# Performance work log

Measured on AMD Instinct MI355X. Metric: run time of the kernel, lower is better.

## Reference

```python
import jax, jax.numpy as jnp
import numpy as np

EPS = 1e-3  # BatchNorm eps (eval mode: running_mean=0, running_var=1)
GRID_D, GRID_H, GRID_W, GRID_C = 10, 400, 352, 128


def bn_last(x, g, b):
    # BatchNorm1d eval over last (channel) axis
    return x * (g / jnp.sqrt(1.0 + EPS)) + b


def bn_ch(x, g, b):
    # BatchNorm3d eval, channel axis 1 of NCDHW
    s = (g / jnp.sqrt(1.0 + EPS)).reshape(1, -1, 1, 1, 1)
    return x * s + b.reshape(1, -1, 1, 1, 1)


def vfe_layer(x, W, g, b):
    # x: [N, T, Cin] -> [N, T, 2*units]
    h = jnp.einsum('ntc,uc->ntu', x, W)
    h = jax.nn.relu(bn_last(h, g, b))
    agg = jnp.max(h, axis=1, keepdims=True)          # [N,1,units]
    return jnp.concatenate([h, jnp.broadcast_to(agg, h.shape)], axis=2)


def pad3(x, p):
    # torch ConstantPad3d order: (Wl, Wr, Hl, Hr, Dl, Dr); x is NCDHW
    return jnp.pad(x, ((0, 0), (0, 0), (p[4], p[5]), (p[2], p[3]), (p[0], p[1])))


def conv3d(x, w, stride):
    return jax.lax.conv_general_dilated(
        x, w, window_strides=stride, padding='VALID',
        dimension_numbers=('NCDHW', 'OIDHW', 'NCDHW'))


def setup_inputs() -> dict:
    key = jax.random.key(0)
    ks = jax.random.split(key, 12)
    N, T = 20000, 35
    features = jax.random.normal(ks[0], (N, T, 4), jnp.float32)
    num_voxels = jax.random.randint(ks[1], (N,), 1, T + 1, jnp.int32)
    cb = jnp.zeros((N, 1), jnp.int32)
    cd = jax.random.randint(ks[2], (N, 1), 0, GRID_D, jnp.int32)
    ch = jax.random.randint(ks[3], (N, 1), 0, GRID_H, jnp.int32)
    cw = jax.random.randint(ks[4], (N, 1), 0, GRID_W, jnp.int32)
    coors = jnp.concatenate([cb, cd, ch, cw], axis=1)

    def lin(k, o, i):
        return jax.random.normal(k, (o, i), jnp.float32) / np.sqrt(i)

    def cw3(k, o, i):
        return jax.random.normal(k, (o, i, 3, 3, 3), jnp.float32) / np.sqrt(i * 27)

    return {
        'features': features, 'num_voxels': num_voxels, 'coors': coors, 'batch_size': 1,
        'w_vfe1': lin(ks[5], 16, 7), 'g_vfe1': jnp.ones(16), 'b_vfe1': jnp.zeros(16),
        'w_vfe2': lin(ks[6], 64, 32), 'g_vfe2': jnp.ones(64), 'b_vfe2': jnp.zeros(64),
        'w_lin': lin(ks[7], 128, 128), 'g_lin': jnp.ones(128), 'b_lin': jnp.zeros(128),
        'w_c1': cw3(ks[8], 64, 128), 'g_c1': jnp.ones(64), 'b_c1': jnp.zeros(64),
        'w_c2': cw3(ks[9], 64, 64), 'g_c2': jnp.ones(64), 'b_c2': jnp.zeros(64),
        'w_c3': cw3(ks[10], 64, 64), 'g_c3': jnp.ones(64), 'b_c3': jnp.zeros(64),
    }


def reference(features, num_voxels, coors, batch_size,
              w_vfe1, g_vfe1, b_vfe1, w_vfe2, g_vfe2, b_vfe2,
              w_lin, g_lin, b_lin,
              w_c1, g_c1, b_c1, w_c2, g_c2, b_c2, w_c3, g_c3, b_c3):
    # --- VoxelFeatureExtractor ---
    nv = num_voxels.astype(features.dtype)[:, None, None]
    points_mean = features[:, :, :3].sum(axis=1, keepdims=True) / nv
    rel = features[:, :, :3] - points_mean
    f = jnp.concatenate([features, rel], axis=-1)                 # [N,T,7]
    T = f.shape[1]
    mask = (jnp.arange(T)[None, :] < num_voxels[:, None]).astype(f.dtype)[..., None]
    x = vfe_layer(f, w_vfe1, g_vfe1, b_vfe1) * mask               # [N,T,32]
    x = vfe_layer(x, w_vfe2, g_vfe2, b_vfe2) * mask               # [N,T,128]
    x = jnp.einsum('ntc,uc->ntu', x, w_lin)
    x = jax.nn.relu(bn_last(x, g_lin, b_lin)) * mask
    voxelwise = jnp.max(x, axis=1)                                # [N,128]

    # --- MiddleExtractor: scatter_nd + 3D convs ---
    grid = jnp.zeros((batch_size, GRID_D, GRID_H, GRID_W, GRID_C), f.dtype)
    grid = grid.at[coors[:, 0], coors[:, 1], coors[:, 2], coors[:, 3]].set(voxelwise)
    r = grid.transpose(0, 4, 1, 2, 3)                             # NCDHW [1,128,10,400,352]
    r = pad3(r, (1, 1, 1, 1, 1, 1))
    r = jax.nn.relu(bn_ch(conv3d(r, w_c1, (2, 1, 1)), g_c1, b_c1))  # [1,64,5,400,352]
    r = pad3(r, (1, 1, 1, 1, 0, 0))
    r = jax.nn.relu(bn_ch(conv3d(r, w_c2, (1, 1, 1)), g_c2, b_c2))  # [1,64,3,400,352]
    r = pad3(r, (1, 1, 1, 1, 1, 1))
    r = jax.nn.relu(bn_ch(conv3d(r, w_c3, (2, 1, 1)), g_c3, b_c3))  # [1,64,2,400,352]
    Nb, C, D, H, W = r.shape
    return r.reshape(Nb, C * D, H, W)                             # [1,128,400,352]
```

## Files before the change

### kernel.cpp

```cpp
#include <hip/hip_runtime.h>
#include <hip/hip_bf16.h>

#define BNC 0.99950037f
#define GH 400
#define GW 352

typedef __bf16 bf16_t;
typedef __bf16 bf16x8 __attribute__((ext_vector_type(8)));
typedef __bf16 bf16x4 __attribute__((ext_vector_type(4)));
typedef float f32x4 __attribute__((ext_vector_type(4)));

__global__ void k_winner(const int* __restrict__ coors, int* __restrict__ winner, int N) {
    int i = blockIdx.x * 256 + threadIdx.x;
    if (i >= N) return;
    int d = coors[i*4+1], h = coors[i*4+2], w = coors[i*4+3];
    atomicMax(&winner[(d*GH + h)*GW + w], i);
}

__global__ void k_tr_w(const float* __restrict__ w, float* __restrict__ wt, int CI, int CO) {
    int idx = blockIdx.x * 256 + threadIdx.x;
    int total = 27 * CI * CO;
    if (idx >= total) return;
    int j   = idx & 3;
    int t1  = idx >> 2;
    int co  = t1 % CO;
    int t2  = t1 / CO;
    int ci4 = t2 % (CI/4);
    int tap = t2 / (CI/4);
    int ci  = ci4*4 + j;
    wt[idx] = w[(co*CI + ci)*27 + tap];
}

__global__ void k_tr_lin(const float* __restrict__ wl, float* __restrict__ WT) {
    int idx = blockIdx.x * 256 + threadIdx.x;
    if (idx >= 16384) return;
    int u = idx & 127, c = idx >> 7;
    WT[c*128 + u] = wl[u*128 + c];
}

__global__ void k_prep(const float* __restrict__ g, const float* __restrict__ b,
                       float* __restrict__ out) {
    int i = threadIdx.x;
    if (i < 64)       out[i] = g[i] * BNC;
    else if (i < 128) out[i] = b[i-64];
}

__global__ void k_packw(const float* __restrict__ w, bf16_t* __restrict__ wh,
                        bf16_t* __restrict__ wlo) {
    int i = blockIdx.x * 256 + threadIdx.x;
    if (i >= 13824) return;
    int lane = i & 63, ct = (i >> 6) & 3, s = i >> 8;
    int tap = s >> 1, h = s & 1;
    int kg = lane >> 4, wl = lane & 15;
    int co = ct*16 + wl;
    #pragma unroll
    for (int j = 0; j < 8; ++j) {
        int ci = h*32 + kg*8 + j;
        float v = w[(co*64 + ci)*27 + tap];
        bf16_t hi = (bf16_t)v;
        wh[(long)i*8 + j]  = hi;
        wlo[(long)i*8 + j] = (bf16_t)(v - (float)hi);
    }
}

__global__ __launch_bounds__(256) void k_vfe(
    const float* __restrict__ feats, const int* __restrict__ nvox,
    const float* __restrict__ w1, const float* __restrict__ g1g, const float* __restrict__ b1g,
    const float* __restrict__ w2g, const float* __restrict__ g2g, const float* __restrict__ b2g,
    const float* __restrict__ WT, const float* __restrict__ glg, const float* __restrict__ blg,
    float* __restrict__ voxelwise, int N)
{
    __shared__ float S[2][4672];
    __shared__ float W1s[16*8];
    __shared__ float SG1[16], SB1[16];

    int tid = threadIdx.x;
    int v   = tid >> 7, lt = tid & 127;
    int vox = blockIdx.x*2 + v;
    if (vox >= N) vox = N - 1;
    int nv  = nvox[vox];

    float* F     = &S[v][0];
    float* X1    = &S[v][280];
    float* X2    = &S[v][980];
    float* RED   = &S[v][3360];
    float* AGG1  = &S[v][4384];
    float* AGG2  = &S[v][4400];
    float* Y2B   = &S[v][4464];
    float* YB    = &S[v][4528];
    float* MEANS = &S[v][4656];

    const float* fsrc = feats + (long)vox * 140;
    for (int idx = lt; idx < 140; idx += 128) { int t = idx>>2, c = idx&3; F[t*8+c] = fsrc[idx]; }
    if (lt < 35) F[lt*8+7] = 0.f;
    if (tid < 112) { int u = tid/7, c = tid - u*7; W1s[u*8+c] = w1[tid]; }
    if (tid < 16)  { W1s[tid*8+7] = 0.f; SG1[tid] = g1g[tid]*BNC; SB1[tid] = b1g[tid]; }
    __syncthreads();

    if (lt < 3) {
        float s = 0.f;
        for (int t = 0; t < 35; ++t) s += F[t*8 + lt];
        MEANS[lt] = s / (float)nv;
    }
    __syncthreads();
    for (int idx = lt; idx < 105; idx += 128) { int t = idx/3, c = idx - t*3; F[t*8+4+c] = F[t*8+c] - MEANS[c]; }
    __syncthreads();

    {
        const float4* Ff4  = (const float4*)F;
        const float4* W1f4 = (const float4*)W1s;
        for (int idx = lt; idx < 560; idx += 128) {
            int t = idx >> 4, u = idx & 15;
            float4 a0 = Ff4[t*2], a1 = Ff4[t*2+1];
            float4 b0 = W1f4[u*2], b1v = W1f4[u*2+1];
            float a = a0.x*b0.x + a0.y*b0.y + a0.z*b0.z + a0.w*b0.w
                    + a1.x*b1v.x + a1.y*b1v.y + a1.z*b1v.z + a1.w*b1v.w;
            X1[t*20+u] = fmaxf(a*SG1[u] + SB1[u], 0.f);
        }
    }
    __syncthreads();
    if (lt < 16) {
        float m = 0.f;
        for (int t = 0; t < 35; ++t) m = fmaxf(m, X1[t*20+lt]);
        AGG1[lt] = m;
    }
    __syncthreads();
    if (lt < 64) {
        const float4* wsrc = (const float4*)(w2g + lt*32 + 16);
        const float4* A1f4 = (const float4*)AGG1;
        float a = 0.f;
        #pragma unroll
        for (int q = 0; q < 4; ++q) {
            float4 w4 = wsrc[q], x4 = A1f4[q];
            a += x4.x*w4.x + x4.y*w4.y + x4.z*w4.z + x4.w*w4.w;
        }
        Y2B[lt] = a;
    }
    __syncthreads();

    {
        int u = lt & 63, tg = lt >> 6;
        float w2r[16];
        const float4* wsrc = (const float4*)(w2g + u*32);
        #pragma unroll
        for (int q = 0; q < 4; ++q) {
            float4 w4 = wsrc[q];
            w2r[q*4] = w4.x; w2r[q*4+1] = w4.y; w2r[q*4+2] = w4.z; w2r[q*4+3] = w4.w;
        }
        float su = g2g[u]*BNC, bu = b2g[u];
        float yb2 = Y2B[u];
        float lm = (nv < 35) ? fmaxf(bu, 0.f) : 0.f;
        for (int t = tg; t < nv; t += 2) {
            const float4* xr = (const float4*)(X1 + t*20);
            float a = yb2;
            #pragma unroll
            for (int q = 0; q < 4; ++q) {
                float4 x4 = xr[q];
                a += x4.x*w2r[q*4] + x4.y*w2r[q*4+1] + x4.z*w2r[q*4+2] + x4.w*w2r[q*4+3];
            }
            float h = fmaxf(a*su + bu, 0.f);
            X2[t*68 + u] = h;
            lm = fmaxf(lm, h);
        }
        RED[tg*64 + u] = lm;
    }
    __syncthreads();
    if (lt < 64) AGG2[lt] = fmaxf(RED[lt], RED[64+lt]);
    __syncthreads();
    {
        float a = 0.f;
        for (int c = 0; c < 64; ++c) a = fmaf(AGG2[c], WT[(64 + c)*128 + lt], a);
        YB[lt] = a;
    }
    __syncthreads();

    {
        int ug = lt & 15, tg4 = lt >> 4;
        int u0 = ug * 8;
        int kmax = (nv > tg4) ? ((nv - tg4 + 7) >> 3) : 0;
        float acc[5][8];
        #pragma unroll
        for (int k = 0; k < 5; ++k)
            #pragma unroll
            for (int j = 0; j < 8; ++j) acc[k][j] = 0.f;

        const float4* X2f4 = (const float4*)X2;
        const float4* WTf4 = (const float4*)WT;
        for (int c4 = 0; c4 < 16; ++c4) {
            float4 wv[8];
            #pragma unroll
            for (int cc = 0; cc < 4; ++cc) {
                wv[cc*2]   = WTf4[(c4*4+cc)*32 + ug*2];
                wv[cc*2+1] = WTf4[(c4*4+cc)*32 + ug*2 + 1];
            }
            #pragma unroll
            for (int k = 0; k < 5; ++k) {
                if (k < kmax) {
                    int t = tg4 + (k << 3);
                    float4 x4 = X2f4[t*17 + c4];
                    #pragma unroll
                    for (int cc = 0; cc < 4; ++cc) {
                        float xs = (cc == 0) ? x4.x : (cc == 1) ? x4.y : (cc == 2) ? x4.z : x4.w;
                        acc[k][0] = fmaf(xs, wv[cc*2].x,   acc[k][0]);
                        acc[k][1] = fmaf(xs, wv[cc*2].y,   acc[k][1]);
                        acc[k][2] = fmaf(xs, wv[cc*2].z,   acc[k][2]);
                        acc[k][3] = fmaf(xs, wv[cc*2].w,   acc[k][3]);
                        acc[k][4] = fmaf(xs, wv[cc*2+1].x, acc[k][4]);
                        acc[k][5] = fmaf(xs, wv[cc*2+1].y, acc[k][5]);
                        acc[k][6] = fmaf(xs, wv[cc*2+1].z, acc[k][6]);
                        acc[k][7] = fmaf(xs, wv[cc*2+1].w, acc[k][7]);
                    }
                }
            }
        }
        float4 g0 = *(const float4*)(glg + u0), g1v = *(const float4*)(glg + u0 + 4);
        float4 b0 = *(const float4*)(blg + u0), b1v = *(const float4*)(blg + u0 + 4);
        float4 y0 = *(const float4*)(YB + u0),  y1v = *(const float4*)(YB + u0 + 4);
        float sg[8] = {g0.x*BNC, g0.y*BNC, g0.z*BNC, g0.w*BNC,
                       g1v.x*BNC, g1v.y*BNC, g1v.z*BNC, g1v.w*BNC};
        float sb[8] = {b0.x, b0.y, b0.z, b0.w, b1v.x, b1v.y, b1v.z, b1v.w};
        float yv[8] = {y0.x, y0.y, y0.z, y0.w, y1v.x, y1v.y, y1v.z, y1v.w};
        float m[8];
        #pragma unroll
        for (int j = 0; j < 8; ++j) m[j] = 0.f;
        #pragma unroll
        for (int k = 0; k < 5; ++k) {
            if (k < kmax) {
                #pragma unroll
                for (int j = 0; j < 8; ++j)
                    m[j] = fmaxf(m[j], fmaxf((acc[k][j] + yv[j])*sg[j] + sb[j], 0.f));
            }
        }
        #pragma unroll
        for (int j = 0; j < 8; ++j) RED[tg4*128 + u0 + j] = m[j];
    }
    __syncthreads();
    {
        float m = RED[lt];
        #pragma unroll
        for (int r = 1; r < 8; ++r) m = fmaxf(m, RED[r*128 + lt]);
        voxelwise[(long)vox*128 + lt] = m;
    }
}

__global__ __launch_bounds__(256) void k_gat1(
    const float4* __restrict__ voxf4, const int* __restrict__ winner,
    const float4* __restrict__ Wt1, bf16_t* __restrict__ accH,
    bf16_t* __restrict__ accL, const float* __restrict__ gact,
    int h_lo, int AR)
{
    int r  = blockIdx.y;
    int oh = h_lo + r;
    if ((unsigned)oh >= (unsigned)GH) return;
    int doo = blockIdx.z;
    int w0  = blockIdx.x * 32;

    __shared__ int sList[306];
    __shared__ int sCnt;
    __shared__ float4 sF[32][32];

    int t = threadIdx.x;
    if (t == 0) sCnt = 0;
    __syncthreads();
    for (int idx = t; idx < 306; idx += 256) {
        int x = idx % 34, q = idx / 34;
        int kd = q / 3, kh = q - kd*3;
        int dp = doo*2 + kd - 1;
        int hp = oh + kh - 1;
        int wp = w0 - 1 + x;
        if ((unsigned)dp < 10u && (unsigned)hp < (unsigned)GH && (unsigned)wp < (unsigned)GW) {
            int v = winner[(dp*GH + hp)*GW + wp];
            if (v >= 0) {
                int p = atomicAdd(&sCnt, 1);
                sList[p] = (v << 10) | (kd << 8) | (kh << 6) | x;
            }
        }
    }
    __syncthreads();
    int cnt = sCnt;

    int co = t & 63, wv = t >> 6;
    int ibase = wv*8;
    float acc[8];
    #pragma unroll
    for (int i = 0; i < 8; ++i) acc[i] = 0.f;

    for (int c0 = 0; c0 < cnt; c0 += 32) {
        int nch = min(32, cnt - c0);
        __syncthreads();
        for (int idx = t; idx < nch*32; idx += 256) {
            int slot = idx >> 5, c = idx & 31;
            int widx = sList[c0 + slot] >> 10;
            sF[slot][c] = voxf4[(long)widx*32 + c];
        }
        __syncthreads();
        for (int e = 0; e < nch; ++e) {
            int ent = sList[c0 + e];
            int x = ent & 63, kh = (ent >> 6) & 3, kd = (ent >> 8) & 3;
            #pragma unroll
            for (int kw = 0; kw < 3; ++kw) {
                int i = x - kw;
                if (i >= ibase && i < ibase + 8) {
                    const float4* wb = Wt1 + (long)(kd*9 + kh*3 + kw)*2048 + co;
                    float a = 0.f;
                    #pragma unroll 4
                    for (int c4 = 0; c4 < 32; ++c4) {
                        float4 wq = wb[c4*64];
                        float4 f4 = sF[e][c4];
                        a += f4.x*wq.x + f4.y*wq.y + f4.z*wq.z + f4.w*wq.w;
                    }
                    int j = i - ibase;
                    #pragma unroll
                    for (int j8 = 0; j8 < 8; ++j8)
                        if (j8 == j) acc[j8] += a;
                }
            }
        }
    }

    float g = gact[co], b = gact[64 + co];
    long rowb = ((long)doo*AR + r)*GW + w0;
    #pragma unroll
    for (int i = 0; i < 8; ++i) {
        float rr = fmaxf(acc[i]*g + b, 0.f);
        bf16_t hi = (bf16_t)rr;
        long idx = (rowb + ibase + i)*64 + co;
        accH[idx] = hi;
        accL[idx] = (bf16_t)(rr - (float)hi);
    }
}

__global__ __launch_bounds__(256) void k_convm(
    const bf16_t* __restrict__ srcH, const bf16_t* __restrict__ srcL,
    int src_h0, long src_dpitch,
    float* __restrict__ dstF, bf16_t* __restrict__ dstH, bf16_t* __restrict__ dstL,
    int dst_h0, long sC, long sD, long sH,
    const bf16_t* __restrict__ wph, const bf16_t* __restrict__ wpl,
    const float* __restrict__ gout, const float* __restrict__ bout,
    int D_in, int d_stride, int d_pad, int y0)
{
    int oh = y0 + (int)blockIdx.y;
    if ((unsigned)oh >= (unsigned)GH) return;

    __shared__ __align__(16) char smem[17408];
    bf16_t* sAh = (bf16_t*)smem;
    bf16_t* sAl = (bf16_t*)(smem + 8448);
    float*  sOut = (float*)smem;

    int t = threadIdx.x;
    int lane = t & 63, wv = t >> 6;
    int wl = lane & 15, kg = lane >> 4;
    int mh = wv >> 1, cth = wv & 1;
    int w0 = (int)blockIdx.x * 64;
    int od = (int)blockIdx.z;

    f32x4 acc[2][2];
    #pragma unroll
    for (int a = 0; a < 2; ++a)
        #pragma unroll
        for (int b = 0; b < 2; ++b) acc[a][b] = (f32x4){0.f, 0.f, 0.f, 0.f};

    const bf16x8* WH = (const bf16x8*)wph;
    const bf16x8* WL = (const bf16x8*)wpl;

    for (int kd = 0; kd < 3; ++kd) {
        int dp = od*d_stride + kd - d_pad;
        if (dp < 0 || dp >= D_in) continue;
        const bf16_t* sdbH = srcH + dp*src_dpitch;
        const bf16_t* sdbL = srcL + dp*src_dpitch;
        for (int kh = 0; kh < 3; ++kh) {
            int hp = oh + kh - 1;
            bool vh = ((unsigned)hp < (unsigned)GH);
            long rowoff = (long)(hp - src_h0) * (GW*64);
            __syncthreads();
            for (int c = t; c < 1056; c += 256) {
                int pl = (c >= 528) ? 1 : 0;
                int cc = c - (pl << 9) - (pl << 4);
                int g = cc / 66, w = cc - g*66;
                int gw = w0 - 1 + w;
                bf16x8 vv;
                if (vh && (unsigned)gw < (unsigned)GW) {
                    const bf16_t* plane = pl ? sdbL : sdbH;
                    vv = *(const bf16x8*)(plane + rowoff + (long)gw*64 + g*8);
                } else {
                    #pragma unroll
                    for (int e = 0; e < 8; ++e) vv[e] = (bf16_t)0.f;
                }
                bf16_t* dstl = pl ? sAl : sAh;
                *(bf16x8*)&dstl[(g*66 + w)*8] = vv;
            }
            __syncthreads();
            #pragma unroll
            for (int h = 0; h < 2; ++h) {
                #pragma unroll
                for (int kw = 0; kw < 3; ++kw) {
                    int s = ((kd*3 + kh)*3 + kw)*2 + h;
                    long fb = (long)(s*4 + cth*2)*64 + lane;
                    bf16x8 B0h = WH[fb],      B0l = WL[fb];
                    bf16x8 B1h = WH[fb + 64], B1l = WL[fb + 64];
                    #pragma unroll
                    for (int mt = 0; mt < 2; ++mt) {
                        int ai = ((h*4 + kg)*66 + (mh*2 + mt)*16 + kw + wl)*8;
                        bf16x8 Ah = *(const bf16x8*)&sAh[ai];
                        bf16x8 Al = *(const bf16x8*)&sAl[ai];
                        acc[mt][0] = __builtin_amdgcn_mfma_f32_16x16x32_bf16(Ah, B0h, acc[mt][0], 0, 0, 0);
                        acc[mt][0] = __builtin_amdgcn_mfma_f32_16x16x32_bf16(Ah, B0l, acc[mt][0], 0, 0, 0);
                        acc[mt][0] = __builtin_amdgcn_mfma_f32_16x16x32_bf16(Al, B0h, acc[mt][0], 0, 0, 0);
                        acc[mt][1] = __builtin_amdgcn_mfma_f32_16x16x32_bf16(Ah, B1h, acc[mt][1], 0, 0, 0);
                        acc[mt][1] = __builtin_amdgcn_mfma_f32_16x16x32_bf16(Ah, B1l, acc[mt][1], 0, 0, 0);
                        acc[mt][1] = __builtin_amdgcn_mfma_f32_16x16x32_bf16(Al, B1h, acc[mt][1], 0, 0, 0);
                    }
                }
            }
        }
    }

    float so[2], bo[2];
    #pragma unroll
    for (int ct = 0; ct < 2; ++ct) {
        int co = (cth*2 + ct)*16 + wl;
        so[ct] = gout[co]*BNC; bo[ct] = bout[co];
    }
    if (dstF) {
        #pragma unroll
        for (int mt = 0; mt < 2; ++mt) {
            int ow = w0 + (mh*2 + mt)*16 + kg*4;
            if (ow < GW) {
                #pragma unroll
                for (int ct = 0; ct < 2; ++ct) {
                    int co = (cth*2 + ct)*16 + wl;
                    f32x4 r;
                    #pragma unroll
                    for (int e = 0; e < 4; ++e)
                        r[e] = fmaxf(acc[mt][ct][e]*so[ct] + bo[ct], 0.f);
                    *(f32x4*)&dstF[(long)co*sC + (long)od*sD + (long)(oh - dst_h0)*sH + ow] = r;
                }
            }
        }
    } else {
        __syncthreads();
        #pragma unroll
        for (int mt = 0; mt < 2; ++mt)
            #pragma unroll
            for (int ct = 0; ct < 2; ++ct) {
                int co = (cth*2 + ct)*16 + wl;
                #pragma unroll
                for (int e = 0; e < 4; ++e) {
                    int owl = (mh*2 + mt)*16 + kg*4 + e;
                    sOut[owl*68 + co] = fmaxf(acc[mt][ct][e]*so[ct] + bo[ct], 0.f);
                }
            }
        __syncthreads();
        for (int f = t; f < 1024; f += 256) {
            int w = f >> 4, c4 = f & 15;
            if (w0 + w < GW) {
                float4 v = *(const float4*)&sOut[w*68 + c4*4];
                long base = (long)od*sD + (long)(oh - dst_h0)*sH + (long)(w0 + w)*64 + c4*4;
                bf16_t h0 = (bf16_t)v.x, h1 = (bf16_t)v.y, h2 = (bf16_t)v.z, h3 = (bf16_t)v.w;
                bf16x4 hv; hv[0]=h0; hv[1]=h1; hv[2]=h2; hv[3]=h3;
                bf16x4 lv;
                lv[0]=(bf16_t)(v.x-(float)h0); lv[1]=(bf16_t)(v.y-(float)h1);
                lv[2]=(bf16_t)(v.z-(float)h2); lv[3]=(bf16_t)(v.w-(float)h3);
                *(bf16x4*)&dstH[base] = hv;
                *(bf16x4*)&dstL[base] = lv;
            }
        }
    }
}

extern "C" void kernel_launch(void* const* d_in, const int* in_sizes, int n_in,
                              void* d_out, int out_size, void* d_ws, size_t ws_size,
                              hipStream_t stream)
{
    const float* feats = (const float*)d_in[0];
    const int*   nvox  = (const int*)d_in[1];
    const int*   coors = (const int*)d_in[2];
    const float* w1  = (const float*)d_in[4];
    const float* g1  = (const float*)d_in[5];
    const float* b1  = (const float*)d_in[6];
    const float* w2  = (const float*)d_in[7];
    const float* g2  = (const float*)d_in[8];
    const float* b2  = (const float*)d_in[9];
    const float* wl  = (const float*)d_in[10];
    const float* gl  = (const float*)d_in[11];
    const float* bl  = (const float*)d_in[12];
    const float* wc1 = (const float*)d_in[13];
    const float* gc1 = (const float*)d_in[14];
    const float* bc1 = (const float*)d_in[15];
    const float* wc2 = (const float*)d_in[16];
    const float* gc2 = (const float*)d_in[17];
    const float* bc2 = (const float*)d_in[18];
    const float* wc3 = (const float*)d_in[19];
    const float* gc3 = (const float*)d_in[20];
    const float* bc3 = (const float*)d_in[21];

    int N = in_sizes[1];

    auto al = [](size_t b) { return (b + 255) & ~(size_t)255; };

    size_t winB = al((size_t)10*GH*GW*4);
    size_t voxB = al((size_t)N*128*4);
    size_t w1B  = al((size_t)27*128*64*4);
    size_t wlB  = al((size_t)128*128*4);
    size_t wpB  = al((size_t)13824*8*2);
    int NS = 20;
    const int cand[8] = {1, 2, 4, 5, 8, 10, 16, 20};
    for (int k = 0; k < 8; ++k) {
        int ns = cand[k], sh = 400/ns, ar = sh + 4, xr = sh + 2;
        size_t tot = 2*al((size_t)5*ar*GW*64*2) + 2*al((size_t)3*xr*GW*64*2)
                   + winB + voxB + w1B + wlB + 4*wpB + 4096;
        if (tot + (1<<16) <= ws_size) { NS = ns; break; }
    }
    int SH = 400/NS, AR = SH + 4, XR = SH + 2;

    char* ws = (char*)d_ws;
    size_t off = 0;
    auto alloc = [&](size_t bytes) -> void* {
        void* p = ws + off; off += al(bytes); return p;
    };
    size_t accB = (size_t)5*AR*GW*64*2;
    size_t actB = (size_t)3*XR*GW*64*2;
    bf16_t* accH   = (bf16_t*)alloc(accB);
    bf16_t* accL   = (bf16_t*)alloc(accB);
    bf16_t* actH   = (bf16_t*)alloc(actB);
    bf16_t* actL   = (bf16_t*)alloc(actB);
    int*    winner = (int*)alloc((size_t)10*GH*GW*4);
    float*  voxw   = (float*)alloc((size_t)N*128*4);
    float*  wt1    = (float*)alloc((size_t)27*128*64*4);
    float*  wtl    = (float*)alloc((size_t)128*128*4);
    bf16_t* wp2h   = (bf16_t*)alloc(wpB);
    bf16_t* wp2l   = (bf16_t*)alloc(wpB);
    bf16_t* wp3h   = (bf16_t*)alloc(wpB);
    bf16_t* wp3l   = (bf16_t*)alloc(wpB);
    float*  gact   = (float*)alloc(256*4);

    hipMemsetAsync(winner, 0xFF, (size_t)10*GH*GW*4, stream);

    k_tr_w<<<(27*128*64 + 255)/256, 256, 0, stream>>>(wc1, wt1, 128, 64);
    k_tr_lin<<<64, 256, 0, stream>>>(wl, wtl);
    k_packw<<<54, 256, 0, stream>>>(wc2, wp2h, wp2l);
    k_packw<<<54, 256, 0, stream>>>(wc3, wp3h, wp3l);
    k_prep<<<1, 256, 0, stream>>>(gc1, bc1, gact);

    k_winner<<<(N + 255)/256, 256, 0, stream>>>(coors, winner, N);
    k_vfe<<<(N + 1)/2, 256, 0, stream>>>(feats, nvox, w1, g1, b1, w2, g2, b2,
                                         wtl, gl, bl, voxw, N);

    for (int s = 0; s < NS; ++s) {
        k_gat1<<<dim3(11, AR, 5), 256, 0, stream>>>(
            (const float4*)voxw, winner, (const float4*)wt1,
            accH, accL, gact, s*SH - 2, AR);
        k_convm<<<dim3(6, SH + 2, 3), 256, 0, stream>>>(
            accH, accL, s*SH - 2, (long)AR*GW*64,
            nullptr, actH, actL, s*SH - 1, 0L, (long)XR*GW*64, (long)GW*64,
            wp2h, wp2l, gc2, bc2,
            5, 1, 0, s*SH - 1);
        k_convm<<<dim3(6, SH, 2), 256, 0, stream>>>(
            actH, actL, s*SH - 1, (long)XR*GW*64,
            (float*)d_out, nullptr, nullptr, 0, (long)2*GH*GW, (long)GH*GW, (long)GW,
            wp3h, wp3l, gc3, bc3,
            3, 2, 1, s*SH);
    }
}
```

Measured before the change: 1.083 ms.

## Compute two output rows per conv block and use one voxel per VFE block

Measured after the change: 1.018 ms. 6.0% less time.

```diff
diff --git a/kernel.cpp b/kernel.cpp
--- a/kernel.cpp
+++ b/kernel.cpp
@@ -63,53 +63,49 @@
     }
 }
 
-__global__ __launch_bounds__(256) void k_vfe(
+__global__ __launch_bounds__(128) void k_vfe(
     const float* __restrict__ feats, const int* __restrict__ nvox,
     const float* __restrict__ w1, const float* __restrict__ g1g, const float* __restrict__ b1g,
     const float* __restrict__ w2g, const float* __restrict__ g2g, const float* __restrict__ b2g,
     const float* __restrict__ WT, const float* __restrict__ glg, const float* __restrict__ blg,
-    float* __restrict__ voxelwise, int N)
+    float* __restrict__ voxelwise)
 {
-    __shared__ float S[2][4672];
+    __shared__ float F[35*8];
     __shared__ float W1s[16*8];
     __shared__ float SG1[16], SB1[16];
+    __shared__ float X1[35*20];
+    __shared__ float X2[35*68];
+    __shared__ float RED[4*128];
+    __shared__ float AGG1[16];
+    __shared__ float AGG2[64];
+    __shared__ float Y2B[64];
+    __shared__ float YB[128];
+    __shared__ float MEANS[3];
 
     int tid = threadIdx.x;
-    int v   = tid >> 7, lt = tid & 127;
-    int vox = blockIdx.x*2 + v;
-    if (vox >= N) vox = N - 1;
+    int vox = blockIdx.x;
     int nv  = nvox[vox];
 
-    float* F     = &S[v][0];
-    float* X1    = &S[v][280];
-    float* X2    = &S[v][980];
-    float* RED   = &S[v][3360];
-    float* AGG1  = &S[v][4384];
-    float* AGG2  = &S[v][4400];
-    float* Y2B   = &S[v][4464];
-    float* YB    = &S[v][4528];
-    float* MEANS = &S[v][4656];
-
     const float* fsrc = feats + (long)vox * 140;
-    for (int idx = lt; idx < 140; idx += 128) { int t = idx>>2, c = idx&3; F[t*8+c] = fsrc[idx]; }
-    if (lt < 35) F[lt*8+7] = 0.f;
+    for (int idx = tid; idx < 140; idx += 128) { int t = idx>>2, c = idx&3; F[t*8+c] = fsrc[idx]; }
+    if (tid < 35) F[tid*8+7] = 0.f;
     if (tid < 112) { int u = tid/7, c = tid - u*7; W1s[u*8+c] = w1[tid]; }
     if (tid < 16)  { W1s[tid*8+7] = 0.f; SG1[tid] = g1g[tid]*BNC; SB1[tid] = b1g[tid]; }
     __syncthreads();
 
-    if (lt < 3) {
+    if (tid < 3) {
         float s = 0.f;
-        for (int t = 0; t < 35; ++t) s += F[t*8 + lt];
-        MEANS[lt] = s / (float)nv;
-    }
-    __syncthreads();
-    for (int idx = lt; idx < 105; idx += 128) { int t = idx/3, c = idx - t*3; F[t*8+4+c] = F[t*8+c] - MEANS[c]; }
+        for (int t = 0; t < 35; ++t) s += F[t*8 + tid];
+        MEANS[tid] = s / (float)nv;
+    }
+    __syncthreads();
+    for (int idx = tid; idx < 105; idx += 128) { int t = idx/3, c = idx - t*3; F[t*8+4+c] = F[t*8+c] - MEANS[c]; }
     __syncthreads();
 
     {
         const float4* Ff4  = (const float4*)F;
         const float4* W1f4 = (const float4*)W1s;
-        for (int idx = lt; idx < 560; idx += 128) {
+        for (int idx = tid; idx < 560; idx += 128) {
             int t = idx >> 4, u = idx & 15;
             float4 a0 = Ff4[t*2], a1 = Ff4[t*2+1];
             float4 b0 = W1f4[u*2], b1v = W1f4[u*2+1];
@@ -119,14 +115,14 @@
         }
     }
     __syncthreads();
-    if (lt < 16) {
+    if (tid < 16) {
         float m = 0.f;
-        for (int t = 0; t < 35; ++t) m = fmaxf(m, X1[t*20+lt]);
-        AGG1[lt] = m;
-    }
-    __syncthreads();
-    if (lt < 64) {
-        const float4* wsrc = (const float4*)(w2g + lt*32 + 16);
+        for (int t = 0; t < 35; ++t) m = fmaxf(m, X1[t*20+tid]);
+        AGG1[tid] = m;
+    }
+    __syncthreads();
+    if (tid < 64) {
+        const float4* wsrc = (const float4*)(w2g + tid*32 + 16);
         const float4* A1f4 = (const float4*)AGG1;
         float a = 0.f;
         #pragma unroll
@@ -134,12 +130,12 @@
             float4 w4 = wsrc[q], x4 = A1f4[q];
             a += x4.x*w4.x + x4.y*w4.y + x4.z*w4.z + x4.w*w4.w;
         }
-        Y2B[lt] = a;
+        Y2B[tid] = a;
     }
     __syncthreads();
 
     {
-        int u = lt & 63, tg = lt >> 6;
+        int u = tid & 63, tg = tid >> 6;
         float w2r[16];
         const float4* wsrc = (const float4*)(w2g + u*32);
         #pragma unroll
@@ -165,81 +161,74 @@
         RED[tg*64 + u] = lm;
     }
     __syncthreads();
-    if (lt < 64) AGG2[lt] = fmaxf(RED[lt], RED[64+lt]);
+    if (tid < 64) AGG2[tid] = fmaxf(RED[tid], RED[64+tid]);
     __syncthreads();
     {
         float a = 0.f;
-        for (int c = 0; c < 64; ++c) a = fmaf(AGG2[c], WT[(64 + c)*128 + lt], a);
-        YB[lt] = a;
+        for (int c = 0; c < 64; ++c) a = fmaf(AGG2[c], WT[(64 + c)*128 + tid], a);
+        YB[tid] = a;
     }
     __syncthreads();
 
     {
-        int ug = lt & 15, tg4 = lt >> 4;
-        int u0 = ug * 8;
-        int kmax = (nv > tg4) ? ((nv - tg4 + 7) >> 3) : 0;
-        float acc[5][8];
-        #pragma unroll
-        for (int k = 0; k < 5; ++k)
-            #pragma unroll
-            for (int j = 0; j < 8; ++j) acc[k][j] = 0.f;
+        int ug = tid & 31, tg4 = tid >> 5;
+        int u0 = ug * 4;
+        int kmax = (nv > tg4) ? ((nv - tg4 + 3) >> 2) : 0;
+        float acc[9][4];
+        #pragma unroll
+        for (int k = 0; k < 9; ++k)
+            #pragma unroll
+            for (int j = 0; j < 4; ++j) acc[k][j] = 0.f;
 
         const float4* X2f4 = (const float4*)X2;
         const float4* WTf4 = (const float4*)WT;
         for (int c4 = 0; c4 < 16; ++c4) {
-            float4 wv[8];
-            #pragma unroll
-            for (int cc = 0; cc < 4; ++cc) {
-                wv[cc*2]   = WTf4[(c4*4+cc)*32 + ug*2];
-                wv[cc*2+1] = WTf4[(c4*4+cc)*32 + ug*2 + 1];
-            }
-            #pragma unroll
-            for (int k = 0; k < 5; ++k) {
+            float4 wv[4];
+            #pragma unroll
+            for (int cc = 0; cc < 4; ++cc)
+                wv[cc] = WTf4[(c4*4+cc)*32 + ug];
+            #pragma unroll
+            for (int k = 0; k < 9; ++k) {
                 if (k < kmax) {
-                    int t = tg4 + (k << 3);
+                    int t = tg4 + (k << 2);
                     float4 x4 = X2f4[t*17 + c4];
                     #pragma unroll
                     for (int cc = 0; cc < 4; ++cc) {
                         float xs = (cc == 0) ? x4.x : (cc == 1) ? x4.y : (cc == 2) ? x4.z : x4.w;
-                        acc[k][0] = fmaf(xs, wv[cc*2].x,   acc[k][0]);
-                        acc[k][1] = fmaf(xs, wv[cc*2].y,   acc[k][1]);
-                        acc[k][2] = fmaf(xs, wv[cc*2].z,   acc[k][2]);
-                        acc[k][3] = fmaf(xs, wv[cc*2].w,   acc[k][3]);
-                        acc[k][4] = fmaf(xs, wv[cc*2+1].x, acc[k][4]);
-                        acc[k][5] = fmaf(xs, wv[cc*2+1].y, acc[k][5]);
-                        acc[k][6] = fmaf(xs, wv[cc*2+1].z, acc[k][6]);
-                        acc[k][7] = fmaf(xs, wv[cc*2+1].w, acc[k][7]);
+                        acc[k][0] = fmaf(xs, wv[cc].x, acc[k][0]);
+                        acc[k][1] = fmaf(xs, wv[cc].y, acc[k][1]);
+                        acc[k][2] = fmaf(xs, wv[cc].z, acc[k][2]);
+                        acc[k][3] = fmaf(xs, wv[cc].w, acc[k][3]);
                     }
                 }
             }
         }
-        float4 g0 = *(const float4*)(glg + u0), g1v = *(const float4*)(glg + u0 + 4);
-        float4 b0 = *(const float4*)(blg + u0), b1v = *(const float4*)(blg + u0 + 4);
-        float4 y0 = *(const float4*)(YB + u0),  y1v = *(const float4*)(YB + u0 + 4);
-        float sg[8] = {g0.x*BNC, g0.y*BNC, g0.z*BNC, g0.w*BNC,
-                       g1v.x*BNC, g1v.y*BNC, g1v.z*BNC, g1v.w*BNC};
-        float sb[8] = {b0.x, b0.y, b0.z, b0.w, b1v.x, b1v.y, b1v.z, b1v.w};
-        float yv[8] = {y0.x, y0.y, y0.z, y0.w, y1v.x, y1v.y, y1v.z, y1v.w};
-        float m[8];
-        #pragma unroll
-        for (int j = 0; j < 8; ++j) m[j] = 0.f;
-        #pragma unroll
-        for (int k = 0; k < 5; ++k) {
+        float4 g0 = *(const float4*)(glg + u0);
+        float4 b0 = *(const float4*)(blg + u0);
+        float4 y0 = *(const float4*)(YB + u0);
+        float sg[4] = {g0.x*BNC, g0.y*BNC, g0.z*BNC, g0.w*BNC};
+        float sb[4] = {b0.x, b0.y, b0.z, b0.w};
+        float yv[4] = {y0.x, y0.y, y0.z, y0.w};
+        float m[4];
+        #pragma unroll
+        for (int j = 0; j < 4; ++j) m[j] = 0.f;
+        #pragma unroll
+        for (int k = 0; k < 9; ++k) {
             if (k < kmax) {
                 #pragma unroll
-                for (int j = 0; j < 8; ++j)
+                for (int j = 0; j < 4; ++j)
                     m[j] = fmaxf(m[j], fmaxf((acc[k][j] + yv[j])*sg[j] + sb[j], 0.f));
             }
         }
         #pragma unroll
-        for (int j = 0; j < 8; ++j) RED[tg4*128 + u0 + j] = m[j];
+        for (int j = 0; j < 4; ++j) RED[tg4*128 + u0 + j] = m[j];
     }
     __syncthreads();
     {
-        float m = RED[lt];
-        #pragma unroll
-        for (int r = 1; r < 8; ++r) m = fmaxf(m, RED[r*128 + lt]);
-        voxelwise[(long)vox*128 + lt] = m;
+        float m = RED[tid];
+        #pragma unroll
+        for (int r = 1; r < 4; ++r) m = fmaxf(m, RED[r*128 + tid]);
+        voxelwise[(long)vox*128 + tid] = m;
     }
 }
 
@@ -337,10 +326,9 @@
     int dst_h0, long sC, long sD, long sH,
     const bf16_t* __restrict__ wph, const bf16_t* __restrict__ wpl,
     const float* __restrict__ gout, const float* __restrict__ bout,
-    int D_in, int d_stride, int d_pad, int y0)
+    int D_in, int d_stride, int d_pad, int y0, int nrows)
 {
-    int oh = y0 + (int)blockIdx.y;
-    if ((unsigned)oh >= (unsigned)GH) return;
+    int oh0 = y0 + (int)blockIdx.y*2;
 
     __shared__ __align__(16) char smem[17408];
     bf16_t* sAh = (bf16_t*)smem;
@@ -354,11 +342,13 @@
     int w0 = (int)blockIdx.x * 64;
     int od = (int)blockIdx.z;
 
-    f32x4 acc[2][2];
+    f32x4 acc[2][2][2];
     #pragma unroll
-    for (int a = 0; a < 2; ++a)
-        #pragma unroll
-        for (int b = 0; b < 2; ++b) acc[a][b] = (f32x4){0.f, 0.f, 0.f, 0.f};
+    for (int o = 0; o < 2; ++o)
+        #pragma unroll
+        for (int a = 0; a < 2; ++a)
+            #pragma unroll
+            for (int b = 0; b < 2; ++b) acc[o][a][b] = (f32x4){0.f, 0.f, 0.f, 0.f};
 
     const bf16x8* WH = (const bf16x8*)wph;
     const bf16x8* WL = (const bf16x8*)wpl;
@@ -368,8 +358,9 @@
         if (dp < 0 || dp >= D_in) continue;
         const bf16_t* sdbH = srcH + dp*src_dpitch;
         const bf16_t* sdbL = srcL + dp*src_dpitch;
-        for (int kh = 0; kh < 3; ++kh) {
-            int hp = oh + kh - 1;
+        #pragma unroll
+        for (int sr = 0; sr < 4; ++sr) {
+            int hp = oh0 - 1 + sr;
             bool vh = ((unsigned)hp < (unsigned)GH);
             long rowoff = (long)(hp - src_h0) * (GW*64);
             __syncthreads();
@@ -378,37 +369,47 @@
                 int cc = c - (pl << 9) - (pl << 4);
                 int g = cc / 66, w = cc - g*66;
                 int gw = w0 - 1 + w;
-                bf16x8 vv;
+                bf16x8 vvv;
                 if (vh && (unsigned)gw < (unsigned)GW) {
                     const bf16_t* plane = pl ? sdbL : sdbH;
-                    vv = *(const bf16x8*)(plane + rowoff + (long)gw*64 + g*8);
+                    vvv = *(const bf16x8*)(plane + rowoff + (long)gw*64 + g*8);
                 } else {
                     #pragma unroll
-                    for (int e = 0; e < 8; ++e) vv[e] = (bf16_t)0.f;
+                    for (int e = 0; e < 8; ++e) vvv[e] = (bf16_t)0.f;
                 }
                 bf16_t* dstl = pl ? sAl : sAh;
-                *(bf16x8*)&dstl[(g*66 + w)*8] = vv;
+                *(bf16x8*)&dstl[(g*66 + w)*8] = vvv;
             }
             __syncthreads();
             #pragma unroll
             for (int h = 0; h < 2; ++h) {
                 #pragma unroll
                 for (int kw = 0; kw < 3; ++kw) {
-                    int s = ((kd*3 + kh)*3 + kw)*2 + h;
-                    long fb = (long)(s*4 + cth*2)*64 + lane;
-                    bf16x8 B0h = WH[fb],      B0l = WL[fb];
-                    bf16x8 B1h = WH[fb + 64], B1l = WL[fb + 64];
+                    bf16x8 Ah[2], Al[2];
                     #pragma unroll
                     for (int mt = 0; mt < 2; ++mt) {
                         int ai = ((h*4 + kg)*66 + (mh*2 + mt)*16 + kw + wl)*8;
-                        bf16x8 Ah = *(const bf16x8*)&sAh[ai];
-                        bf16x8 Al = *(const bf16x8*)&sAl[ai];
-                        acc[mt][0] = __builtin_amdgcn_mfma_f32_16x16x32_bf16(Ah, B0h, acc[mt][0], 0, 0, 0);
-                        acc[mt][0] = __builtin_amdgcn_mfma_f32_16x16x32_bf16(Ah, B0l, acc[mt][0], 0, 0, 0);
-                        acc[mt][0] = __builtin_amdgcn_mfma_f32_16x16x32_bf16(Al, B0h, acc[mt][0], 0, 0, 0);
-                        acc[mt][1] = __builtin_amdgcn_mfma_f32_16x16x32_bf16(Ah, B1h, acc[mt][1], 0, 0, 0);
-                        acc[mt][1] = __builtin_amdgcn_mfma_f32_16x16x32_bf16(Ah, B1l, acc[mt][1], 0, 0, 0);
-                        acc[mt][1] = __builtin_amdgcn_mfma_f32_16x16x32_bf16(Al, B1h, acc[mt][1], 0, 0, 0);
+                        Ah[mt] = *(const bf16x8*)&sAh[ai];
+                        Al[mt] = *(const bf16x8*)&sAl[ai];
+                    }
+                    #pragma unroll
+                    for (int oi = 0; oi < 2; ++oi) {
+                        int kh = sr - oi;
+                        if (kh >= 0 && kh < 3) {
+                            int s = ((kd*3 + kh)*3 + kw)*2 + h;
+                            long fb = (long)(s*4 + cth*2)*64 + lane;
+                            bf16x8 B0h = WH[fb],      B0l = WL[fb];
+                            bf16x8 B1h = WH[fb + 64], B1l = WL[fb + 64];
+                            #pragma unroll
+                            for (int mt = 0; mt < 2; ++mt) {
+                                acc[oi][mt][0] = __builtin_amdgcn_mfma_f32_16x16x32_bf16(Ah[mt], B0h, acc[oi][mt][0], 0, 0, 0);
+                                acc[oi][mt][0] = __builtin_amdgcn_mfma_f32_16x16x32_bf16(Ah[mt], B0l, acc[oi][mt][0], 0, 0, 0);
+                                acc[oi][mt][0] = __builtin_amdgcn_mfma_f32_16x16x32_bf16(Al[mt], B0h, acc[oi][mt][0], 0, 0, 0);
+                                acc[oi][mt][1] = __builtin_amdgcn_mfma_f32_16x16x32_bf16(Ah[mt], B1h, acc[oi][mt][1], 0, 0, 0);
+                                acc[oi][mt][1] = __builtin_amdgcn_mfma_f32_16x16x32_bf16(Ah[mt], B1l, acc[oi][mt][1], 0, 0, 0);
+                                acc[oi][mt][1] = __builtin_amdgcn_mfma_f32_16x16x32_bf16(Al[mt], B1h, acc[oi][mt][1], 0, 0, 0);
+                            }
+                        }
                     }
                 }
             }
@@ -423,46 +424,61 @@
     }
     if (dstF) {
         #pragma unroll
-        for (int mt = 0; mt < 2; ++mt) {
-            int ow = w0 + (mh*2 + mt)*16 + kg*4;
-            if (ow < GW) {
+        for (int oi = 0; oi < 2; ++oi) {
+            int oh = oh0 + oi;
+            bool rv = ((unsigned)oh < (unsigned)GH) && ((int)blockIdx.y*2 + oi < nrows);
+            if (rv) {
                 #pragma unroll
-                for (int ct = 0; ct < 2; ++ct) {
-                    int co = (cth*2 + ct)*16 + wl;
-                    f32x4 r;
-                    #pragma unroll
-                    for (int e = 0; e < 4; ++e)
-                        r[e] = fmaxf(acc[mt][ct][e]*so[ct] + bo[ct], 0.f);
-                    *(f32x4*)&dstF[(long)co*sC + (long)od*sD + (long)(oh - dst_h0)*sH + ow] = r;
+                for (int mt = 0; mt < 2; ++mt) {
+                    int ow = w0 + (mh*2 + mt)*16 + kg*4;
+                    if (ow < GW) {
+                        #pragma unroll
+                        for (int ct = 0; ct < 2; ++ct) {
+                            int co = (cth*2 + ct)*16 + wl;
+                            f32x4 r;
+                            #pragma unroll
+                            for (int e = 0; e < 4; ++e)
+                                r[e] = fmaxf(acc[oi][mt][ct][e]*so[ct] + bo[ct], 0.f);
+                            *(f32x4*)&dstF[(long)co*sC + (long)od*sD + (long)(oh - dst_h0)*sH + ow] = r;
+                        }
+                    }
                 }
             }
         }
     } else {
         __syncthreads();
         #pragma unroll
-        for (int mt = 0; mt < 2; ++mt)
-            #pragma unroll
-            for (int ct = 0; ct < 2; ++ct) {
-                int co = (cth*2 + ct)*16 + wl;
+        for (int oi = 0; oi < 2; ++oi) {
+            int oh = oh0 + oi;
+            bool rv = ((unsigned)oh < (unsigned)GH) && ((int)blockIdx.y*2 + oi < nrows);
+            if (rv) {
                 #pragma unroll
-                for (int e = 0; e < 4; ++e) {
-                    int owl = (mh*2 + mt)*16 + kg*4 + e;
-                    sOut[owl*68 + co] = fmaxf(acc[mt][ct][e]*so[ct] + bo[ct], 0.f);
+                for (int mt = 0; mt < 2; ++mt)
+                    #pragma unroll
+                    for (int ct = 0; ct < 2; ++ct) {
+                        int co = (cth*2 + ct)*16 + wl;
+                        #pragma unroll
+                        for (int e = 0; e < 4; ++e) {
+                            int owl = (mh*2 + mt)*16 + kg*4 + e;
+                            sOut[owl*68 + co] = fmaxf(acc[oi][mt][ct][e]*so[ct] + bo[ct], 0.f);
+                        }
+                    }
+                __syncthreads();
+                for (int f = t; f < 1024; f += 256) {
+                    int w = f >> 4, c4 = f & 15;
+                    if (w0 + w < GW) {
+                        float4 v = *(const float4*)&sOut[w*68 + c4*4];
+                        long base = (long)od*sD + (long)(oh - dst_h0)*sH + (long)(w0 + w)*64 + c4*4;
+                        bf16_t h0 = (bf16_t)v.x, h1 = (bf16_t)v.y, h2 = (bf16_t)v.z, h3 = (bf16_t)v.w;
+                        bf16x4 hv; hv[0]=h0; hv[1]=h1; hv[2]=h2; hv[3]=h3;
+                        bf16x4 lv;
+                        lv[0]=(bf16_t)(v.x-(float)h0); lv[1]=(bf16_t)(v.y-(float)h1);
+                        lv[2]=(bf16_t)(v.z-(float)h2); lv[3]=(bf16_t)(v.w-(float)h3);
+                        *(bf16x4*)&dstH[base] = hv;
+                        *(bf16x4*)&dstL[base] = lv;
+                    }
                 }
-            }
-        __syncthreads();
-        for (int f = t; f < 1024; f += 256) {
-            int w = f >> 4, c4 = f & 15;
-            if (w0 + w < GW) {
-                float4 v = *(const float4*)&sOut[w*68 + c4*4];
-                long base = (long)od*sD + (long)(oh - dst_h0)*sH + (long)(w0 + w)*64 + c4*4;
-                bf16_t h0 = (bf16_t)v.x, h1 = (bf16_t)v.y, h2 = (bf16_t)v.z, h3 = (bf16_t)v.w;
-                bf16x4 hv; hv[0]=h0; hv[1]=h1; hv[2]=h2; hv[3]=h3;
-                bf16x4 lv;
-                lv[0]=(bf16_t)(v.x-(float)h0); lv[1]=(bf16_t)(v.y-(float)h1);
-                lv[2]=(bf16_t)(v.z-(float)h2); lv[3]=(bf16_t)(v.w-(float)h3);
-                *(bf16x4*)&dstH[base] = hv;
-                *(bf16x4*)&dstL[base] = lv;
+                __syncthreads();
             }
         }
     }
@@ -543,22 +559,22 @@
     k_prep<<<1, 256, 0, stream>>>(gc1, bc1, gact);
 
     k_winner<<<(N + 255)/256, 256, 0, stream>>>(coors, winner, N);
-    k_vfe<<<(N + 1)/2, 256, 0, stream>>>(feats, nvox, w1, g1, b1, w2, g2, b2,
-                                         wtl, gl, bl, voxw, N);
+    k_vfe<<<N, 128, 0, stream>>>(feats, nvox, w1, g1, b1, w2, g2, b2,
+                                 wtl, gl, bl, voxw);
 
     for (int s = 0; s < NS; ++s) {
         k_gat1<<<dim3(11, AR, 5), 256, 0, stream>>>(
             (const float4*)voxw, winner, (const float4*)wt1,
             accH, accL, gact, s*SH - 2, AR);
-        k_convm<<<dim3(6, SH + 2, 3), 256, 0, stream>>>(
+        k_convm<<<dim3(6, (SH + 2 + 1)/2, 3), 256, 0, stream>>>(
             accH, accL, s*SH - 2, (long)AR*GW*64,
             nullptr, actH, actL, s*SH - 1, 0L, (long)XR*GW*64, (long)GW*64,
             wp2h, wp2l, gc2, bc2,
-            5, 1, 0, s*SH - 1);
-        k_convm<<<dim3(6, SH, 2), 256, 0, stream>>>(
+            5, 1, 0, s*SH - 1, SH + 2);
+        k_convm<<<dim3(6, (SH + 1)/2, 2), 256, 0, stream>>>(
             actH, actL, s*SH - 1, (long)XR*GW*64,
             (float*)d_out, nullptr, nullptr, 0, (long)2*GH*GW, (long)GH*GW, (long)GW,
             wp3h, wp3l, gc3, bc3,
-            3, 2, 1, s*SH);
-    }
-}
+            3, 2, 1, s*SH, SH);
+    }
+}
```
